# Kernel tuning notes

Hardware: AMD Instinct MI355X
Metric: run time of the kernel (lower is better)

The kernel has to match this reference:

```python
import jax, jax.numpy as jnp
import numpy as np

UNITS = 1024
OUT_STEPS = 200
SEQ_LEN = 5
NUM_FEATURES = 1
BATCH = 4096


def _lstm_cell(x, h, c, kernel, recurrent_kernel, bias):
    # Keras LSTMCell: z = x@K + h@R + b, gates in order i, f, g(candidate), o
    z = x @ kernel + h @ recurrent_kernel + bias  # [B, 4U]
    i, f, g, o = jnp.split(z, 4, axis=-1)
    i = jax.nn.sigmoid(i)
    f = jax.nn.sigmoid(f)
    g = jnp.tanh(g)
    o = jax.nn.sigmoid(o)
    c_new = f * c + i * g
    h_new = o * jnp.tanh(c_new)
    return h_new, c_new


def setup_inputs() -> dict:
    key = jax.random.key(0)
    ks = jax.random.split(key, 8)
    s = 0.05  # modest init scale to keep gates unsaturated
    return {
        "inputs": jax.random.normal(ks[0], (BATCH, SEQ_LEN, NUM_FEATURES), jnp.float32),
        "kernel": jax.random.normal(ks[1], (NUM_FEATURES, 4 * UNITS), jnp.float32) * s,
        "recurrent_kernel": jax.random.normal(ks[2], (UNITS, 4 * UNITS), jnp.float32) * s,
        "bias": jax.random.normal(ks[3], (4 * UNITS,), jnp.float32) * s,
        "w1": jax.random.normal(ks[4], (UNITS, NUM_FEATURES), jnp.float32) * s,
        "b1": jax.random.normal(ks[5], (NUM_FEATURES,), jnp.float32) * s,
        "w2": jax.random.normal(ks[6], (NUM_FEATURES, NUM_FEATURES), jnp.float32) * s,
        "b2": jax.random.normal(ks[7], (NUM_FEATURES,), jnp.float32) * s,
    }


def reference(inputs, kernel, recurrent_kernel, bias, w1, b1, w2, b2):
    B = inputs.shape[0]
    h0 = jnp.zeros((B, UNITS), inputs.dtype)
    c0 = jnp.zeros((B, UNITS), inputs.dtype)

    # warmup: run LSTM over the input sequence (lax.scan over time)
    def warm_step(carry, x_t):
        h, c = carry
        h, c = _lstm_cell(x_t, h, c, kernel, recurrent_kernel, bias)
        return (h, c), None

    (h, c), _ = jax.lax.scan(warm_step, (h0, c0), jnp.swapaxes(inputs, 0, 1))
    pred0 = jax.nn.relu(h @ w1 + b1)  # first prediction: dense1 only (per warmup())

    def dec_step(carry, _):
        pred, h, c = carry
        h, c = _lstm_cell(pred, h, c, kernel, recurrent_kernel, bias)
        x = jax.nn.relu(h @ w1 + b1)
        pred = x @ w2 + b2
        return (pred, h, c), pred

    _, preds = jax.lax.scan(dec_step, (pred0, h, c), None, length=OUT_STEPS - 1)
    # preds: [T-1, B, F] -> stack with pred0 and transpose to [B, T, F]
    all_preds = jnp.concatenate([pred0[None], preds], axis=0)
    return jnp.transpose(all_preds, (1, 0, 2))
```

## Files before the change

### kernel.cpp

```cpp
#include <hip/hip_runtime.h>
#include <hip/hip_bf16.h>
#include <stdint.h>
#include <stddef.h>

#define B_SZ   4096
#define U_SZ   1024
#define SEQ    5
#define TSTEPS 200
#define STEPS  204

typedef __bf16 bf16_t;
typedef __bf16 bf16x8 __attribute__((ext_vector_type(8)));
typedef float  f32x4  __attribute__((ext_vector_type(4)));

#define AS1 __attribute__((address_space(1)))
#define AS3 __attribute__((address_space(3)))

#define LOAD_LDS16(gp, lp) \
    __builtin_amdgcn_global_load_lds((const AS1 unsigned int*)(gp), \
                                     (AS3 unsigned int*)(lp), 16, 0, 0)

__device__ __forceinline__ float fsig(float x) {
    return 1.0f / (1.0f + __expf(-x));
}
__device__ __forceinline__ float ftanh(float x) {
    x = fminf(fmaxf(x, -15.0f), 15.0f);
    float e = __expf(2.0f * x);
    return (e - 1.0f) / (e + 1.0f);
}

__global__ void pack_R(const float* __restrict__ R, bf16_t* __restrict__ Rp) {
    int idx = blockIdx.x * 256 + threadIdx.x;
    int kk = idx & 63;
    int c  = (idx >> 6) & 127;
    int kb = (idx >> 13) & 15;
    int ub = idx >> 17;
    int g  = (c >> 4) & 3;
    int wc = c >> 6;
    int cl = c & 15;
    int n  = g * 1024 + ub * 32 + wc * 16 + cl;
    int k  = kb * 64 + kk;
    Rp[idx] = (bf16_t)R[(size_t)k * 4096 + n];
}

__global__ __launch_bounds__(256, 2)
void lstm_step(const bf16_t* __restrict__ hin,
               bf16_t* __restrict__ hout,
               float* __restrict__ cst,
               const bf16_t* __restrict__ Rp,
               const float* __restrict__ Wx,
               const float* __restrict__ bias,
               const float* __restrict__ w1,
               const float* __restrict__ b1,
               const float* __restrict__ w2,
               const float* __restrict__ b2,
               const float* __restrict__ inputs,
               float* __restrict__ praw,
               float* __restrict__ out,
               int t)
{
    __shared__ __align__(16) bf16_t lsA[128 * 64];
    __shared__ __align__(16) bf16_t lsB[2][128 * 64];
    __shared__ float lsX[128];

    const int tid  = threadIdx.x;
    const int wave = tid >> 6;
    const int lane = tid & 63;
    const int p    = blockIdx.x;
    const int G    = blockIdx.y;
    const int l15  = lane & 15;
    const int quad = lane >> 4;
    const int rbase = (wave >> 1) * 64;
    const int wc    = wave & 1;

    float*       pr_acc  = praw + (size_t)(t % 3) * B_SZ;
    const float* pr_read = praw + (size_t)((t + 2) % 3) * B_SZ;
    float*       pr_zero = praw + (size_t)((t + 1) % 3) * B_SZ;

    if (tid < 128) {
        int row = G * 128 + tid;
        float x;
        if (t < SEQ) {
            x = inputs[row * SEQ + t];
        } else {
            float x1 = fmaxf(pr_read[row] + b1[0], 0.f);
            x = (t == SEQ) ? x1 : x1 * w2[0] + b2[0];
            if (p == 0) out[(size_t)row * TSTEPS + (t - SEQ)] = x;
        }
        lsX[tid] = x;
        if (p == 0) pr_zero[row] = 0.f;
    }

    f32x4 acc[2][4][4] = {};
    const bf16_t* Ap  = hin + (size_t)G * 128 * U_SZ;
    const bf16_t* Bp0 = Rp + (size_t)(2 * p) * 131072;
    const bf16_t* Bp1 = Bp0 + 131072;

    for (int kb = 0; kb < 16; ++kb) {
        #pragma unroll
        for (int i = 0; i < 4; ++i) {
            int chunk = wave * 4 + i;
            int m  = chunk * 8 + (lane >> 3);
            int kk = (lane & 7) * 8;
            LOAD_LDS16(Ap + (size_t)m * U_SZ + kb * 64 + kk, &lsA[chunk * 512]);
        }
        #pragma unroll
        for (int i = 0; i < 4; ++i) {
            int chunk = wave * 4 + i;
            LOAD_LDS16(Bp0 + (size_t)kb * 8192 + chunk * 512 + lane * 8,
                       &lsB[0][chunk * 512]);
            LOAD_LDS16(Bp1 + (size_t)kb * 8192 + chunk * 512 + lane * 8,
                       &lsB[1][chunk * 512]);
        }
        __syncthreads();

        #pragma unroll
        for (int kh = 0; kh < 2; ++kh) {
            int ko = kh * 32 + quad * 8;
            bf16x8 af[4];
            #pragma unroll
            for (int mi = 0; mi < 4; ++mi)
                af[mi] = *(const bf16x8*)&lsA[(rbase + mi * 16 + l15) * 64 + ko];
            #pragma unroll
            for (int T = 0; T < 2; ++T) {
                bf16x8 bfr[4];
                #pragma unroll
                for (int ni = 0; ni < 4; ++ni)
                    bfr[ni] = *(const bf16x8*)
                        &lsB[T][(wc * 64 + ni * 16 + l15) * 64 + ko];
                #pragma unroll
                for (int mi = 0; mi < 4; ++mi)
                    #pragma unroll
                    for (int ni = 0; ni < 4; ++ni)
                        acc[T][mi][ni] = __builtin_amdgcn_mfma_f32_16x16x32_bf16(
                            af[mi], bfr[ni], acc[T][mi][ni], 0, 0, 0);
            }
        }
        __syncthreads();
    }

    int uu[2];
    uu[0] = (2 * p) * 32 + wc * 16 + l15;
    uu[1] = uu[0] + 32;
    float g_b[2][4], g_w[2][4], w1u[2];
    #pragma unroll
    for (int T = 0; T < 2; ++T) {
        #pragma unroll
        for (int g = 0; g < 4; ++g) {
            g_b[T][g] = bias[g * 1024 + uu[T]];
            g_w[T][g] = Wx[g * 1024 + uu[T]];
        }
        w1u[T] = w1[uu[T]];
    }
    const bool do_pred = (t >= SEQ - 1);

    #pragma unroll
    for (int mi = 0; mi < 4; ++mi) {
        #pragma unroll
        for (int r = 0; r < 4; ++r) {
            int rl   = rbase + mi * 16 + quad * 4 + r;
            int brow = G * 128 + rl;
            float xv = lsX[rl];
            float ps = 0.f;
            #pragma unroll
            for (int T = 0; T < 2; ++T) {
                float zi = acc[T][mi][0][r] + g_b[T][0] + xv * g_w[T][0];
                float zf = acc[T][mi][1][r] + g_b[T][1] + xv * g_w[T][1];
                float zg = acc[T][mi][2][r] + g_b[T][2] + xv * g_w[T][2];
                float zo = acc[T][mi][3][r] + g_b[T][3] + xv * g_w[T][3];
                float ig = fsig(zi), fg = fsig(zf);
                float gg = ftanh(zg), og = fsig(zo);
                size_t off = (size_t)brow * U_SZ + uu[T];
                float cn = fg * cst[off] + ig * gg;
                cst[off] = cn;
                float hv = og * ftanh(cn);
                hout[off] = (bf16_t)hv;
                ps += hv * w1u[T];
            }
            if (do_pred) {
                ps += __shfl_xor(ps, 1);
                ps += __shfl_xor(ps, 2);
                ps += __shfl_xor(ps, 4);
                ps += __shfl_xor(ps, 8);
                if (l15 == 0) atomicAdd(&pr_acc[brow], ps);
            }
        }
    }
}

__global__ void pred_final(const float* __restrict__ praw,
                           const float* __restrict__ b1,
                           const float* __restrict__ w2,
                           const float* __restrict__ b2,
                           float* __restrict__ out)
{
    int row = blockIdx.x * 256 + threadIdx.x;
    float x1 = fmaxf(praw[2 * B_SZ + row] + b1[0], 0.f);
    out[(size_t)row * TSTEPS + 199] = x1 * w2[0] + b2[0];
}

extern "C" void kernel_launch(void* const* d_in, const int* in_sizes, int n_in,
                              void* d_out, int out_size, void* d_ws, size_t ws_size,
                              hipStream_t stream) {
    const float* inputs = (const float*)d_in[0];
    const float* Wx     = (const float*)d_in[1];
    const float* R      = (const float*)d_in[2];
    const float* bias   = (const float*)d_in[3];
    const float* w1     = (const float*)d_in[4];
    const float* b1     = (const float*)d_in[5];
    const float* w2     = (const float*)d_in[6];
    const float* b2     = (const float*)d_in[7];
    float* out = (float*)d_out;

    char* ws = (char*)d_ws;
    const size_t RP_BYTES = (size_t)32 * 131072 * 2;
    const size_t H_BYTES  = (size_t)B_SZ * U_SZ * 2;
    const size_t C_BYTES  = (size_t)B_SZ * U_SZ * 4;
    bf16_t* Rp   = (bf16_t*)ws;                ws += RP_BYTES;
    bf16_t* h0   = (bf16_t*)ws;                ws += H_BYTES;
    bf16_t* h1   = (bf16_t*)ws;                ws += H_BYTES;
    float*  cbuf = (float*)ws;                 ws += C_BYTES;
    float*  praw = (float*)ws;                 ws += 3 * B_SZ * 4;
    bf16_t* hb[2] = {h0, h1};

    hipMemsetAsync(h0, 0, H_BYTES, stream);
    hipMemsetAsync(cbuf, 0, C_BYTES, stream);
    hipMemsetAsync(praw, 0, 3 * B_SZ * 4, stream);

    pack_R<<<16384, 256, 0, stream>>>(R, Rp);

    dim3 grid(16, 32);
    int cur = 0;
    for (int t = 0; t < STEPS; ++t) {
        lstm_step<<<grid, 256, 0, stream>>>(hb[cur], hb[1 - cur], cbuf, Rp,
                                            Wx, bias, w1, b1, w2, b2,
                                            inputs, praw, out, t);
        cur ^= 1;
    }
    pred_final<<<16, 256, 0, stream>>>(praw, b1, w2, b2, out);
}
```

Before: 10.06 ms.

## Double-buffer A tile in LDS with swizzle, load B fragments directly from global

Moves the recurrent-weight (B) operand out of LDS: each wave now reads its MFMA fragments straight from global memory into registers. The h (A) tile is double-buffered in LDS, so the next k-block is prefetched while the current one is computed, and it is stored with an XOR swizzle to reduce bank conflicts. This cuts LDS footprint and leaves one barrier per iteration instead of two. The cost is exposed global-load latency on B, relying on cache hits.

```diff
diff --git a/kernel.cpp b/kernel.cpp
--- a/kernel.cpp
+++ b/kernel.cpp
@@ -59,8 +59,7 @@
                float* __restrict__ out,
                int t)
 {
-    __shared__ __align__(16) bf16_t lsA[128 * 64];
-    __shared__ __align__(16) bf16_t lsB[2][128 * 64];
+    __shared__ __align__(16) bf16_t lsA[2][128 * 64];
     __shared__ float lsX[128];
 
     const int tid  = threadIdx.x;
@@ -96,46 +95,75 @@
     const bf16_t* Bp0 = Rp + (size_t)(2 * p) * 131072;
     const bf16_t* Bp1 = Bp0 + 131072;
 
+    const int a_kk = (((lane & 7) ^ (lane >> 3)) << 3);
+    const int a_m  = lane >> 3;
+
+    const int bOff = (wc * 64 + l15) * 64 + quad * 8;
+
+    #pragma unroll
+    for (int i = 0; i < 4; ++i) {
+        int chunk = wave * 4 + i;
+        LOAD_LDS16(Ap + (size_t)(chunk * 8 + a_m) * U_SZ + a_kk,
+                   &lsA[0][chunk * 512]);
+    }
+    __syncthreads();
+
+    #pragma unroll 2
     for (int kb = 0; kb < 16; ++kb) {
-        #pragma unroll
-        for (int i = 0; i < 4; ++i) {
-            int chunk = wave * 4 + i;
-            int m  = chunk * 8 + (lane >> 3);
-            int kk = (lane & 7) * 8;
-            LOAD_LDS16(Ap + (size_t)m * U_SZ + kb * 64 + kk, &lsA[chunk * 512]);
-        }
-        #pragma unroll
-        for (int i = 0; i < 4; ++i) {
-            int chunk = wave * 4 + i;
-            LOAD_LDS16(Bp0 + (size_t)kb * 8192 + chunk * 512 + lane * 8,
-                       &lsB[0][chunk * 512]);
-            LOAD_LDS16(Bp1 + (size_t)kb * 8192 + chunk * 512 + lane * 8,
-                       &lsB[1][chunk * 512]);
-        }
-        __syncthreads();
-
+        const bf16_t* lsAc = lsA[kb & 1];
+        const bf16_t* Bk0 = Bp0 + (size_t)kb * 8192 + bOff;
+        const bf16_t* Bk1 = Bp1 + (size_t)kb * 8192 + bOff;
+
+        bf16x8 bfr[2][4];
+        #pragma unroll
+        for (int ni = 0; ni < 4; ++ni) {
+            bfr[0][ni] = *(const bf16x8*)(Bk0 + ni * 1024);
+            bfr[1][ni] = *(const bf16x8*)(Bk1 + ni * 1024);
+        }
+
+        if (kb < 15) {
+            #pragma unroll
+            for (int i = 0; i < 4; ++i) {
+                int chunk = wave * 4 + i;
+                LOAD_LDS16(Ap + (size_t)(chunk * 8 + a_m) * U_SZ
+                               + (kb + 1) * 64 + a_kk,
+                           &lsA[(kb + 1) & 1][chunk * 512]);
+            }
+        }
+
+        bf16x8 af[2][4];
         #pragma unroll
         for (int kh = 0; kh < 2; ++kh) {
-            int ko = kh * 32 + quad * 8;
-            bf16x8 af[4];
+            int sw = (((kh * 4 + quad) ^ (lane & 7)) << 3);
             #pragma unroll
             for (int mi = 0; mi < 4; ++mi)
-                af[mi] = *(const bf16x8*)&lsA[(rbase + mi * 16 + l15) * 64 + ko];
-            #pragma unroll
-            for (int T = 0; T < 2; ++T) {
-                bf16x8 bfr[4];
+                af[kh][mi] =
+                    *(const bf16x8*)&lsAc[(rbase + mi * 16 + l15) * 64 + sw];
+        }
+
+        #pragma unroll
+        for (int T = 0; T < 2; ++T)
+            #pragma unroll
+            for (int mi = 0; mi < 4; ++mi)
                 #pragma unroll
                 for (int ni = 0; ni < 4; ++ni)
-                    bfr[ni] = *(const bf16x8*)
-                        &lsB[T][(wc * 64 + ni * 16 + l15) * 64 + ko];
+                    acc[T][mi][ni] = __builtin_amdgcn_mfma_f32_16x16x32_bf16(
+                        af[0][mi], bfr[T][ni], acc[T][mi][ni], 0, 0, 0);
+
+        #pragma unroll
+        for (int ni = 0; ni < 4; ++ni) {
+            bfr[0][ni] = *(const bf16x8*)(Bk0 + 32 + ni * 1024);
+            bfr[1][ni] = *(const bf16x8*)(Bk1 + 32 + ni * 1024);
+        }
+        #pragma unroll
+        for (int T = 0; T < 2; ++T)
+            #pragma unroll
+            for (int mi = 0; mi < 4; ++mi)
                 #pragma unroll
-                for (int mi = 0; mi < 4; ++mi)
-                    #pragma unroll
-                    for (int ni = 0; ni < 4; ++ni)
-                        acc[T][mi][ni] = __builtin_amdgcn_mfma_f32_16x16x32_bf16(
-                            af[mi], bfr[ni], acc[T][mi][ni], 0, 0, 0);
-            }
-        }
+                for (int ni = 0; ni < 4; ++ni)
+                    acc[T][mi][ni] = __builtin_amdgcn_mfma_f32_16x16x32_bf16(
+                        af[1][mi], bfr[T][ni], acc[T][mi][ni], 0, 0, 0);
+
         __syncthreads();
     }
 
```

Result: slower. 16.48 ms (+63.7%).
